# Optimization experiments

Measured on AMD Instinct MI355X. Metric: run time of the kernel, lower is better.

Reference implementation:

```python
import jax, jax.numpy as jnp
import numpy as np

N = 50000          # nodes
E = 800000         # edges (before self-loops)
D_IN, D_H, D_OUT = 128, 256, 256
SZ_C = 2           # channels
NUM_GRAPHS = 64
EPS = 1e-6


def setup_inputs() -> dict:
    key = jax.random.key(0)
    ks = jax.random.split(key, 12)
    x = jax.random.normal(ks[0], (N, D_IN), dtype=jnp.float32)
    edge = jax.random.randint(ks[1], (2, E), 0, N, dtype=jnp.int64)
    batch = jnp.sort(jax.random.randint(ks[2], (N,), 0, NUM_GRAPHS, dtype=jnp.int64))
    def glorot(k, shape):
        fan = shape[-2] + shape[-1]
        return jax.random.normal(k, shape, dtype=jnp.float32) * jnp.sqrt(2.0 / fan)
    W0 = glorot(ks[3], (SZ_C, D_IN, D_H)); b0 = jnp.zeros((SZ_C, D_H), jnp.float32)
    W1 = glorot(ks[4], (SZ_C, D_H, D_H));  b1 = jnp.zeros((SZ_C, D_H), jnp.float32)
    W2 = glorot(ks[5], (SZ_C, D_H, D_OUT)); b2 = jnp.zeros((SZ_C, D_OUT), jnp.float32)
    ln_w = jnp.ones((D_OUT,), jnp.float32)
    ln_b = jnp.zeros((D_OUT,), jnp.float32)
    return {"x": x, "edge": edge, "batch": batch,
            "W0": W0, "b0": b0, "W1": W1, "b1": b1, "W2": W2, "b2": b2,
            "ln_w": ln_w, "ln_b": ln_b}


def _gcn_conv(h, W, b, src, dst, norm):
    # PyG GCNConv: linear transform, then deg-normalized scatter-add, then bias
    h = h @ W                                  # [N, d_out]
    msg = h[src] * norm[:, None]               # [E+N, d_out] gathered messages
    agg = jax.ops.segment_sum(msg, dst, num_segments=N)
    return agg + b


def reference(x, edge, batch, W0, b0, W1, b1, W2, b2, ln_w, ln_b):
    # add self-loops (GCNConv default add_self_loops=True)
    loops = jnp.arange(N, dtype=edge.dtype)
    src = jnp.concatenate([edge[0], loops])
    dst = jnp.concatenate([edge[1], loops])
    # symmetric normalization: deg^{-1/2}[src] * deg^{-1/2}[dst], deg over targets
    deg = jax.ops.segment_sum(jnp.ones_like(dst, dtype=x.dtype), dst, num_segments=N)
    dinv = jnp.where(deg > 0, jax.lax.rsqrt(deg), 0.0)
    norm = dinv[src] * dinv[dst]

    channels = []
    for c in range(SZ_C):  # small fixed channel count
        h = x
        for (W, b) in ((W0[c], b0[c]), (W1[c], b1[c]), (W2[c], b2[c])):
            h = _gcn_conv(h, W, b, src, dst, norm)
            h = jax.nn.relu(h) + h  # residual: ReLU output + pre-ReLU input
        channels.append(h)
    channal = jnp.stack(channels)              # [sz_c, N, d_out]

    mean = channal.mean(-1, keepdims=True)
    var = channal.var(-1, keepdims=True)
    out = (channal - mean) * jax.lax.rsqrt(var + EPS) * ln_w + ln_b

    batchs = jnp.ones((SZ_C, 1), channal.dtype) * batch.astype(channal.dtype)[None, :]
    return out, batchs
```

## Files before the change

kernel.cpp:

```cpp
#include <hip/hip_runtime.h>
#include <hip/hip_bf16.h>

typedef __bf16 v8bf __attribute__((ext_vector_type(8)));
typedef float  v4f  __attribute__((ext_vector_type(4)));
typedef float  v2f  __attribute__((ext_vector_type(2)));

constexpr int N_NODES = 50000;
constexpr int N_EDGES = 800000;
constexpr float LN_EPS = 1e-6f;
constexpr int ROW_TILES = N_NODES / 16;

#define ACC_FP8X8(w, a)                                              \
  {                                                                  \
    v2f p0 = __builtin_amdgcn_cvt_pk_f32_fp8((w).x, false);          \
    v2f p1 = __builtin_amdgcn_cvt_pk_f32_fp8((w).x, true);           \
    v2f p2 = __builtin_amdgcn_cvt_pk_f32_fp8((w).y, false);          \
    v2f p3 = __builtin_amdgcn_cvt_pk_f32_fp8((w).y, true);           \
    a[0] += p0.x; a[1] += p0.y; a[2] += p1.x; a[3] += p1.y;          \
    a[4] += p2.x; a[5] += p2.y; a[6] += p3.x; a[7] += p3.y;          \
  }

__device__ __forceinline__ unsigned char f32_to_fp8(float v) {
  int pk = __builtin_amdgcn_cvt_pk_fp8_f32(v, v, 0, false);
  return (unsigned char)(pk & 0xFF);
}

__global__ void probe_kernel(const int* __restrict__ edge, int* __restrict__ flag) {
  int t = threadIdx.x;
  int nz = 0;
  for (int i = t * 2 + 1; i < 4096; i += 128) nz |= (edge[i] != 0);
  unsigned long long m = __ballot(nz);
  if (t == 0) flag[0] = (m == 0ull) ? 1 : 0;
}

__device__ __forceinline__ int ld_idx(const void* base, int i, int is64) {
  int v;
  if (is64) v = (int)((const long long*)base)[(long long)i];
  else      v = ((const int*)base)[i];
  if ((unsigned)v >= (unsigned)N_NODES) v = 0;
  return v;
}


__global__ void init_kernel(int* __restrict__ deg, int* __restrict__ gcount) {
  int i = blockIdx.x * 256 + threadIdx.x;
  if (i < N_NODES) deg[i] = 1;
  if (i == 0) gcount[0] = 0;
}

__global__ void count_kernel(const void* __restrict__ edge, const int* __restrict__ flag,
                             int* __restrict__ deg) {
  int e = blockIdx.x * 256 + threadIdx.x;
  if (e < N_EDGES) atomicAdd(&deg[ld_idx(edge, N_EDGES + e, flag[0])], 1);
}

__global__ __launch_bounds__(256) void block_offsets_kernel(
    const int* __restrict__ deg, int* __restrict__ gcount,
    int* __restrict__ rowstart, int* __restrict__ cursor, float* __restrict__ dinv) {
  __shared__ int ps[256];
  __shared__ int base_s;
  int tid = threadIdx.x;
  int node = blockIdx.x * 256 + tid;
  int d = (node < N_NODES) ? deg[node] : 1;
  int cnt = d - 1;
  ps[tid] = cnt;
  __syncthreads();
#pragma unroll
  for (int off = 1; off < 256; off <<= 1) {
    int v = (tid >= off) ? ps[tid - off] : 0;
    __syncthreads();
    ps[tid] += v;
    __syncthreads();
  }
  if (tid == 255) base_s = atomicAdd(gcount, ps[255]);
  __syncthreads();
  int start = base_s + ps[tid] - cnt;
  if (node < N_NODES) {
    rowstart[node] = start;
    cursor[node]   = start;
    dinv[node]     = rsqrtf((float)max(d, 1));
  }
}

__global__ void scatter_kernel(const void* __restrict__ edge, const int* __restrict__ flag,
                               int* __restrict__ cursor, int* __restrict__ csr_src) {
  int e = blockIdx.x * 256 + threadIdx.x;
  if (e >= N_EDGES) return;
  int f = flag[0];
  int s = ld_idx(edge, e, f);
  int d = ld_idx(edge, N_EDGES + e, f);
  int pos = atomicAdd(&cursor[d], 1);
  if ((unsigned)pos < (unsigned)N_EDGES) csr_src[pos] = s;
}

__global__ void pack_all_kernel(const float* __restrict__ W0, const float* __restrict__ W1,
                                const float* __restrict__ W2, __bf16* __restrict__ Wp) {
  int tid = blockIdx.x * 256 + threadIdx.x;
  const float* src; int local;
  if (tid < 65536)       { src = W0 + (size_t)(tid >> 15) * (128 * 256); local = tid & 32767; }
  else if (tid < 196608) { int t2 = tid - 65536;  src = W1 + (size_t)(t2 >> 16) * 65536; local = t2 & 65535; }
  else                   { int t2 = tid - 196608; src = W2 + (size_t)(t2 >> 16) * 65536; local = t2 & 65535; }
  int j    = local & 7;
  int lane = (local >> 3) & 63;
  int ct   = (local >> 9) & 15;
  int kc   = local >> 13;
  int k    = kc * 32 + ((lane >> 4) << 3) + j;
  int col  = ct * 16 + (lane & 15);
  Wp[tid] = (__bf16)src[k * 256 + col];
}

__global__ __launch_bounds__(256) void prescale_x_kernel(
    const float* __restrict__ x, const float* __restrict__ dinv, __bf16* __restrict__ xd) {
  int t = blockIdx.x * 256 + threadIdx.x;
  int node = t >> 4;
  int d0 = (t & 15) * 8;
  float di = dinv[node];
  v4f f0 = *(const v4f*)(x + (size_t)node * 128 + d0);
  v4f f1 = *(const v4f*)(x + (size_t)node * 128 + d0 + 4);
  v8bf o;
#pragma unroll
  for (int j = 0; j < 4; j++) { o[j] = (__bf16)(di * f0[j]); o[4 + j] = (__bf16)(di * f1[j]); }
  *(v8bf*)(xd + (size_t)node * 128 + d0) = o;
}

__global__ __launch_bounds__(256) void fused0_kernel(
    const __bf16* __restrict__ Yd, const int* __restrict__ rowstart,
    const int* __restrict__ deg, const int* __restrict__ csr_src,
    const float* __restrict__ dinv, const __bf16* __restrict__ Wp,
    const float* __restrict__ bias,
    unsigned char* __restrict__ Hd) {
  __shared__ __bf16 lds[16 * 128];
  __shared__ int wcnt;
  char* lb = (char*)lds;
  int wave = threadIdx.x >> 6;
  int lane = threadIdx.x & 63;
  int sub = lane >> 4;
  int dc = (lane & 15) * 8;
  if (threadIdx.x == 0) wcnt = 0;
  __syncthreads();

  for (;;) {
    int row;
    if (lane == 0) row = atomicAdd(&wcnt, 1);
    row = __shfl(row, 0);
    if (row >= 16) break;
    int node = blockIdx.x * 16 + row;

    int start = rowstart[node];
    int cnt = deg[node] - 1;
    start = max(0, min(start, N_EDGES));
    cnt = max(0, min(cnt, N_EDGES - start));
    int e = start, end = start + cnt;

    float di = dinv[node];
    v8bf ys = *(const v8bf*)(Yd + (unsigned)(node * 128 + dc));

    float a[8];
#pragma unroll
    for (int j = 0; j < 8; j++) a[j] = 0.f;

    for (; e + 16 <= end; e += 16) {
      int s0 = csr_src[e + sub];
      int s1 = csr_src[e + 4 + sub];
      int s2 = csr_src[e + 8 + sub];
      int s3 = csr_src[e + 12 + sub];
      if ((unsigned)s0 >= (unsigned)N_NODES) s0 = 0;
      if ((unsigned)s1 >= (unsigned)N_NODES) s1 = 0;
      if ((unsigned)s2 >= (unsigned)N_NODES) s2 = 0;
      if ((unsigned)s3 >= (unsigned)N_NODES) s3 = 0;
      v8bf y0 = *(const v8bf*)(Yd + (unsigned)(s0 * 128 + dc));
      v8bf y1 = *(const v8bf*)(Yd + (unsigned)(s1 * 128 + dc));
      v8bf y2 = *(const v8bf*)(Yd + (unsigned)(s2 * 128 + dc));
      v8bf y3 = *(const v8bf*)(Yd + (unsigned)(s3 * 128 + dc));
#pragma unroll
      for (int j = 0; j < 8; j++)
        a[j] += ((float)y0[j] + (float)y1[j]) + ((float)y2[j] + (float)y3[j]);
    }
    if (e + 8 <= end) {
      int s0 = csr_src[e + sub];
      int s1 = csr_src[e + 4 + sub];
      if ((unsigned)s0 >= (unsigned)N_NODES) s0 = 0;
      if ((unsigned)s1 >= (unsigned)N_NODES) s1 = 0;
      v8bf y0 = *(const v8bf*)(Yd + (unsigned)(s0 * 128 + dc));
      v8bf y1 = *(const v8bf*)(Yd + (unsigned)(s1 * 128 + dc));
#pragma unroll
      for (int j = 0; j < 8; j++) a[j] += (float)y0[j] + (float)y1[j];
      e += 8;
    }
    if (e + 4 <= end) {
      int s0 = csr_src[e + sub];
      if ((unsigned)s0 >= (unsigned)N_NODES) s0 = 0;
      v8bf y0 = *(const v8bf*)(Yd + (unsigned)(s0 * 128 + dc));
#pragma unroll
      for (int j = 0; j < 8; j++) a[j] += (float)y0[j];
      e += 4;
    }
    int rem = end - e;
    if (sub < rem) {
      int s0 = csr_src[e + sub];
      if ((unsigned)s0 >= (unsigned)N_NODES) s0 = 0;
      v8bf y0 = *(const v8bf*)(Yd + (unsigned)(s0 * 128 + dc));
#pragma unroll
      for (int j = 0; j < 8; j++) a[j] += (float)y0[j];
    }

#pragma unroll
    for (int off = 16; off < 64; off <<= 1)
#pragma unroll
      for (int j = 0; j < 8; j++) a[j] += __shfl_xor(a[j], off);

    if (sub == 0) {
      v8bf u;
#pragma unroll
      for (int j = 0; j < 8; j++) u[j] = (__bf16)(di * (a[j] + (float)ys[j]));
      int byte = (row * 256 + dc * 2) ^ ((row & 7) << 4);
      *(v8bf*)(lb + byte) = u;
    }
  }
  __syncthreads();

  int ch = wave >> 1, q = wave & 1;
  const __bf16* Wsec = Wp + ch * 32768;
  const float* bch = bias + ch * 256;
  int arow = lane & 15;
  int g = lane >> 4;

  v8bf af[4];
#pragma unroll
  for (int kc = 0; kc < 4; kc++) {
    int byte = (arow * 256 + g * 16 + kc * 64) ^ ((arow & 7) << 4);
    af[kc] = *(const v8bf*)(lb + byte);
  }

  int crow = blockIdx.x * 16 + (g << 2);
  float dv[4];
#pragma unroll
  for (int r = 0; r < 4; r++) dv[r] = dinv[crow + r];

#pragma unroll
  for (int c4 = 0; c4 < 8; c4++) {
    int ct = q * 8 + c4;
    v8bf bf[4];
#pragma unroll
    for (int kc = 0; kc < 4; kc++)
      bf[kc] = *(const v8bf*)(Wsec + (size_t)((kc * 16 + ct) * 64 + lane) * 8);
    v4f acc = (v4f){0.f, 0.f, 0.f, 0.f};
#pragma unroll
    for (int kc = 0; kc < 4; kc++)
      acc = __builtin_amdgcn_mfma_f32_16x16x32_bf16(af[kc], bf[kc], acc, 0, 0, 0);
    int wcol = ct * 16 + (lane & 15);
    float bb = bch[wcol];
#pragma unroll
    for (int r = 0; r < 4; r++) {
      float z = acc[r] + bb;
      float h = z + fmaxf(z, 0.f);
      Hd[(size_t)(crow + r) * 512 + ch * 256 + wcol] = f32_to_fp8(dv[r] * h);
    }
  }
}

__global__ __launch_bounds__(256) void fusedA_kernel(
    const unsigned char* __restrict__ A,
    const int* __restrict__ rowstart, const int* __restrict__ deg,
    const int* __restrict__ csr_src, const float* __restrict__ dinv,
    const __bf16* __restrict__ Wp,
    const float* __restrict__ bias,
    unsigned char* __restrict__ Hd) {
  __shared__ __bf16 lds[16 * 512];
  __shared__ int wcnt;
  char* lb = (char*)lds;
  int wave = threadIdx.x >> 6;
  int lane = threadIdx.x & 63;
  unsigned lb8 = (unsigned)(lane * 8);
  if (threadIdx.x == 0) wcnt = 0;
  __syncthreads();

  for (;;) {
    int row;
    if (lane == 0) row = atomicAdd(&wcnt, 1);
    row = __shfl(row, 0);
    if (row >= 16) break;
    int node = blockIdx.x * 16 + row;

    int start = rowstart[node];
    int cnt = deg[node] - 1;
    start = max(0, min(start, N_EDGES));
    cnt = max(0, min(cnt, N_EDGES - start));
    int e = start, end = start + cnt;

    float di = dinv[node];
    uint2 wys = *(const uint2*)(A + (unsigned)(node * 512) + lb8);

    float a[8];
#pragma unroll
    for (int j = 0; j < 8; j++) a[j] = 0.f;

    for (; e + 8 <= end; e += 8) {
      int s0 = csr_src[e],     s1 = csr_src[e + 1];
      int s2 = csr_src[e + 2], s3 = csr_src[e + 3];
      int s4 = csr_src[e + 4], s5 = csr_src[e + 5];
      int s6 = csr_src[e + 6], s7 = csr_src[e + 7];
      if ((unsigned)s0 >= (unsigned)N_NODES) s0 = 0;
      if ((unsigned)s1 >= (unsigned)N_NODES) s1 = 0;
      if ((unsigned)s2 >= (unsigned)N_NODES) s2 = 0;
      if ((unsigned)s3 >= (unsigned)N_NODES) s3 = 0;
      if ((unsigned)s4 >= (unsigned)N_NODES) s4 = 0;
      if ((unsigned)s5 >= (unsigned)N_NODES) s5 = 0;
      if ((unsigned)s6 >= (unsigned)N_NODES) s6 = 0;
      if ((unsigned)s7 >= (unsigned)N_NODES) s7 = 0;
      uint2 w0 = *(const uint2*)(A + (unsigned)(s0 * 512) + lb8);
      uint2 w1 = *(const uint2*)(A + (unsigned)(s1 * 512) + lb8);
      uint2 w2 = *(const uint2*)(A + (unsigned)(s2 * 512) + lb8);
      uint2 w3 = *(const uint2*)(A + (unsigned)(s3 * 512) + lb8);
      uint2 w4 = *(const uint2*)(A + (unsigned)(s4 * 512) + lb8);
      uint2 w5 = *(const uint2*)(A + (unsigned)(s5 * 512) + lb8);
      uint2 w6 = *(const uint2*)(A + (unsigned)(s6 * 512) + lb8);
      uint2 w7 = *(const uint2*)(A + (unsigned)(s7 * 512) + lb8);
      ACC_FP8X8(w0, a); ACC_FP8X8(w1, a); ACC_FP8X8(w2, a); ACC_FP8X8(w3, a);
      ACC_FP8X8(w4, a); ACC_FP8X8(w5, a); ACC_FP8X8(w6, a); ACC_FP8X8(w7, a);
    }
    if (e + 4 <= end) {
      int s0 = csr_src[e],     s1 = csr_src[e + 1];
      int s2 = csr_src[e + 2], s3 = csr_src[e + 3];
      if ((unsigned)s0 >= (unsigned)N_NODES) s0 = 0;
      if ((unsigned)s1 >= (unsigned)N_NODES) s1 = 0;
      if ((unsigned)s2 >= (unsigned)N_NODES) s2 = 0;
      if ((unsigned)s3 >= (unsigned)N_NODES) s3 = 0;
      uint2 w0 = *(const uint2*)(A + (unsigned)(s0 * 512) + lb8);
      uint2 w1 = *(const uint2*)(A + (unsigned)(s1 * 512) + lb8);
      uint2 w2 = *(const uint2*)(A + (unsigned)(s2 * 512) + lb8);
      uint2 w3 = *(const uint2*)(A + (unsigned)(s3 * 512) + lb8);
      ACC_FP8X8(w0, a); ACC_FP8X8(w1, a); ACC_FP8X8(w2, a); ACC_FP8X8(w3, a);
      e += 4;
    }
    for (; e < end; e++) {
      int s0 = csr_src[e];
      if ((unsigned)s0 >= (unsigned)N_NODES) s0 = 0;
      uint2 w0 = *(const uint2*)(A + (unsigned)(s0 * 512) + lb8);
      ACC_FP8X8(w0, a);
    }

    float ysf[8];
    {
      v2f q0 = __builtin_amdgcn_cvt_pk_f32_fp8(wys.x, false);
      v2f q1 = __builtin_amdgcn_cvt_pk_f32_fp8(wys.x, true);
      v2f q2 = __builtin_amdgcn_cvt_pk_f32_fp8(wys.y, false);
      v2f q3 = __builtin_amdgcn_cvt_pk_f32_fp8(wys.y, true);
      ysf[0] = q0.x; ysf[1] = q0.y; ysf[2] = q1.x; ysf[3] = q1.y;
      ysf[4] = q2.x; ysf[5] = q2.y; ysf[6] = q3.x; ysf[7] = q3.y;
    }
    v8bf u;
#pragma unroll
    for (int j = 0; j < 8; j++) u[j] = (__bf16)(di * (a[j] + ysf[j]));
    int byte = (row * 1024 + lane * 16) ^ ((row & 7) << 4);
    *(v8bf*)(lb + byte) = u;
  }
  __syncthreads();

  int ch = wave >> 1, q = wave & 1;
  const __bf16* Wsec = Wp + ch * 65536;
  const float* bch = bias + ch * 256;
  int arow = lane & 15;
  int g = lane >> 4;

  v8bf af[8];
#pragma unroll
  for (int kc = 0; kc < 8; kc++) {
    int byte = (arow * 1024 + ch * 512 + g * 16 + kc * 64) ^ ((arow & 7) << 4);
    af[kc] = *(const v8bf*)(lb + byte);
  }

  int crow = blockIdx.x * 16 + (g << 2);
  float dv[4];
#pragma unroll
  for (int r = 0; r < 4; r++) dv[r] = dinv[crow + r];

#pragma unroll
  for (int c4 = 0; c4 < 8; c4++) {
    int ct = q * 8 + c4;
    v8bf bf[8];
#pragma unroll
    for (int kc = 0; kc < 8; kc++)
      bf[kc] = *(const v8bf*)(Wsec + (size_t)((kc * 16 + ct) * 64 + lane) * 8);
    v4f acc = (v4f){0.f, 0.f, 0.f, 0.f};
#pragma unroll
    for (int kc = 0; kc < 8; kc++)
      acc = __builtin_amdgcn_mfma_f32_16x16x32_bf16(af[kc], bf[kc], acc, 0, 0, 0);
    int wcol = ct * 16 + (lane & 15);
    float bb = bch[wcol];
#pragma unroll
    for (int r = 0; r < 4; r++) {
      float z = acc[r] + bb;
      float h = z + fmaxf(z, 0.f);
      Hd[(size_t)(crow + r) * 512 + ch * 256 + wcol] = f32_to_fp8(dv[r] * h);
    }
  }
}

__global__ __launch_bounds__(256) void agg_fp8_kernel(
    const unsigned char* __restrict__ A, const int* __restrict__ rowstart,
    const int* __restrict__ deg, const int* __restrict__ csr_src,
    const float* __restrict__ dinv, __bf16* __restrict__ U) {
  int node = blockIdx.x * 4 + (threadIdx.x >> 6);
  int lane = threadIdx.x & 63;
  unsigned lb8 = (unsigned)(lane * 8);

  int start = rowstart[node];
  int cnt = deg[node] - 1;
  start = max(0, min(start, N_EDGES));
  cnt = max(0, min(cnt, N_EDGES - start));
  int e = start, end = start + cnt;

  float di = dinv[node];
  uint2 wys = *(const uint2*)(A + (unsigned)(node * 512) + lb8);

  float a[8];
#pragma unroll
  for (int j = 0; j < 8; j++) a[j] = 0.f;

  for (; e + 8 <= end; e += 8) {
    int s0 = csr_src[e],     s1 = csr_src[e + 1];
    int s2 = csr_src[e + 2], s3 = csr_src[e + 3];
    int s4 = csr_src[e + 4], s5 = csr_src[e + 5];
    int s6 = csr_src[e + 6], s7 = csr_src[e + 7];
    if ((unsigned)s0 >= (unsigned)N_NODES) s0 = 0;
    if ((unsigned)s1 >= (unsigned)N_NODES) s1 = 0;
    if ((unsigned)s2 >= (unsigned)N_NODES) s2 = 0;
    if ((unsigned)s3 >= (unsigned)N_NODES) s3 = 0;
    if ((unsigned)s4 >= (unsigned)N_NODES) s4 = 0;
    if ((unsigned)s5 >= (unsigned)N_NODES) s5 = 0;
    if ((unsigned)s6 >= (unsigned)N_NODES) s6 = 0;
    if ((unsigned)s7 >= (unsigned)N_NODES) s7 = 0;
    uint2 w0 = *(const uint2*)(A + (unsigned)(s0 * 512) + lb8);
    uint2 w1 = *(const uint2*)(A + (unsigned)(s1 * 512) + lb8);
    uint2 w2 = *(const uint2*)(A + (unsigned)(s2 * 512) + lb8);
    uint2 w3 = *(const uint2*)(A + (unsigned)(s3 * 512) + lb8);
    uint2 w4 = *(const uint2*)(A + (unsigned)(s4 * 512) + lb8);
    uint2 w5 = *(const uint2*)(A + (unsigned)(s5 * 512) + lb8);
    uint2 w6 = *(const uint2*)(A + (unsigned)(s6 * 512) + lb8);
    uint2 w7 = *(const uint2*)(A + (unsigned)(s7 * 512) + lb8);
    ACC_FP8X8(w0, a); ACC_FP8X8(w1, a); ACC_FP8X8(w2, a); ACC_FP8X8(w3, a);
    ACC_FP8X8(w4, a); ACC_FP8X8(w5, a); ACC_FP8X8(w6, a); ACC_FP8X8(w7, a);
  }
  if (e + 4 <= end) {
    int s0 = csr_src[e],     s1 = csr_src[e + 1];
    int s2 = csr_src[e + 2], s3 = csr_src[e + 3];
    if ((unsigned)s0 >= (unsigned)N_NODES) s0 = 0;
    if ((unsigned)s1 >= (unsigned)N_NODES) s1 = 0;
    if ((unsigned)s2 >= (unsigned)N_NODES) s2 = 0;
    if ((unsigned)s3 >= (unsigned)N_NODES) s3 = 0;
    uint2 w0 = *(const uint2*)(A + (unsigned)(s0 * 512) + lb8);
    uint2 w1 = *(const uint2*)(A + (unsigned)(s1 * 512) + lb8);
    uint2 w2 = *(const uint2*)(A + (unsigned)(s2 * 512) + lb8);
    uint2 w3 = *(const uint2*)(A + (unsigned)(s3 * 512) + lb8);
    ACC_FP8X8(w0, a); ACC_FP8X8(w1, a); ACC_FP8X8(w2, a); ACC_FP8X8(w3, a);
    e += 4;
  }
  for (; e < end; e++) {
    int s0 = csr_src[e];
    if ((unsigned)s0 >= (unsigned)N_NODES) s0 = 0;
    uint2 w0 = *(const uint2*)(A + (unsigned)(s0 * 512) + lb8);
    ACC_FP8X8(w0, a);
  }

  float ysf[8];
  {
    v2f q0 = __builtin_amdgcn_cvt_pk_f32_fp8(wys.x, false);
    v2f q1 = __builtin_amdgcn_cvt_pk_f32_fp8(wys.x, true);
    v2f q2 = __builtin_amdgcn_cvt_pk_f32_fp8(wys.y, false);
    v2f q3 = __builtin_amdgcn_cvt_pk_f32_fp8(wys.y, true);
    ysf[0] = q0.x; ysf[1] = q0.y; ysf[2] = q1.x; ysf[3] = q1.y;
    ysf[4] = q2.x; ysf[5] = q2.y; ysf[6] = q3.x; ysf[7] = q3.y;
  }
  v8bf u;
#pragma unroll
  for (int j = 0; j < 8; j++) u[j] = (__bf16)(di * (a[j] + ysf[j]));
  *(v8bf*)(U + (unsigned)(node * 512) + (unsigned)(lane * 8)) = u;
}

__global__ __launch_bounds__(256, 2) void gemm_final_kernel(
    const __bf16* __restrict__ A, const __bf16* __restrict__ Wp,
    const float* __restrict__ bias, const float* __restrict__ lnw,
    const float* __restrict__ lnb, float* __restrict__ out) {
  constexpr int KC = 8;
  constexpr int LDA = 512;
  __shared__ float ls1[4][16];
  __shared__ float ls2[4][16];
  int lane = threadIdx.x & 63;
  int wave = threadIdx.x >> 6;

  v8bf bfrag[KC][4];
#pragma unroll
  for (int kc = 0; kc < KC; kc++)
#pragma unroll
    for (int c4 = 0; c4 < 4; c4++)
      bfrag[kc][c4] = *(const v8bf*)(Wp + ((size_t)((kc * 16 + wave * 4 + c4) * 64 + lane)) * 8);

  int arow = lane & 15;
  int akq = (lane >> 4) * 8;
  int g = lane >> 4;
  int ccol = wave * 64 + (lane & 15);
  float bcol[4], wcol[4], lbcol[4];
#pragma unroll
  for (int c4 = 0; c4 < 4; c4++) {
    int col = ccol + c4 * 16;
    bcol[c4] = bias[col];
    wcol[c4] = lnw[col];
    lbcol[c4] = lnb[col];
  }

  for (int t = blockIdx.x; t < ROW_TILES; t += gridDim.x) {
    int row0 = t * 16;
    const __bf16* Ap = A + (size_t)(row0 + arow) * LDA + akq;
    v8bf af[KC];
#pragma unroll
    for (int kc = 0; kc < KC; kc++) af[kc] = *(const v8bf*)(Ap + kc * 32);

    v4f acc[4];
#pragma unroll
    for (int c4 = 0; c4 < 4; c4++) acc[c4] = (v4f){0.f, 0.f, 0.f, 0.f};
#pragma unroll
    for (int kc = 0; kc < KC; kc++)
#pragma unroll
      for (int c4 = 0; c4 < 4; c4++)
        acc[c4] = __builtin_amdgcn_mfma_f32_16x16x32_bf16(af[kc], bfrag[kc][c4], acc[c4], 0, 0, 0);

    float h[4][4];
#pragma unroll
    for (int c4 = 0; c4 < 4; c4++)
#pragma unroll
      for (int r = 0; r < 4; r++) {
        float z = acc[c4][r] + bcol[c4];
        h[c4][r] = z + fmaxf(z, 0.f);
      }

    float s1[4], s2[4];
#pragma unroll
    for (int r = 0; r < 4; r++) {
      s1[r] = 0.f; s2[r] = 0.f;
#pragma unroll
      for (int c4 = 0; c4 < 4; c4++) { s1[r] += h[c4][r]; s2[r] += h[c4][r] * h[c4][r]; }
    }
#pragma unroll
    for (int off = 1; off < 16; off <<= 1)
#pragma unroll
      for (int r = 0; r < 4; r++) {
        s1[r] += __shfl_xor(s1[r], off);
        s2[r] += __shfl_xor(s2[r], off);
      }
    if ((lane & 15) == 0) {
#pragma unroll
      for (int r = 0; r < 4; r++) { ls1[wave][g * 4 + r] = s1[r]; ls2[wave][g * 4 + r] = s2[r]; }
    }
    __syncthreads();
#pragma unroll
    for (int r = 0; r < 4; r++) {
      int row = g * 4 + r;
      float t1 = ls1[0][row] + ls1[1][row] + ls1[2][row] + ls1[3][row];
      float t2 = ls2[0][row] + ls2[1][row] + ls2[2][row] + ls2[3][row];
      float mean = t1 * (1.0f / 256.0f);
      float var = t2 * (1.0f / 256.0f) - mean * mean;
      float rstd = rsqrtf(fmaxf(var, 0.f) + LN_EPS);
#pragma unroll
      for (int c4 = 0; c4 < 4; c4++)
        out[(size_t)(row0 + row) * 256 + ccol + c4 * 16] =
            (h[c4][r] - mean) * rstd * wcol[c4] + lbcol[c4];
    }
    __syncthreads();
  }
}

__global__ void batchs_kernel(const void* __restrict__ batch, const int* __restrict__ flag,
                              float* __restrict__ ob) {
  int i = blockIdx.x * 256 + threadIdx.x;
  if (i >= N_NODES) return;
  int f = flag[0];
  int v;
  if (f) v = (int)((const long long*)batch)[i];
  else   v = ((const int*)batch)[i];
  float b = (float)v;
  ob[i] = b;
  ob[N_NODES + i] = b;
}


extern "C" void kernel_launch(void* const* d_in, const int* in_sizes, int n_in,
                              void* d_out, int out_size, void* d_ws, size_t ws_size,
                              hipStream_t stream) {
  const float* x    = (const float*)d_in[0];
  const void*  edge = d_in[1];
  const void*  batch= d_in[2];
  const float* W0   = (const float*)d_in[3];
  const float* b0   = (const float*)d_in[4];
  const float* W1   = (const float*)d_in[5];
  const float* b1   = (const float*)d_in[6];
  const float* W2   = (const float*)d_in[7];
  const float* b2   = (const float*)d_in[8];
  const float* lnw  = (const float*)d_in[9];
  const float* lnb  = (const float*)d_in[10];

  float* out_x = (float*)d_out;
  float* out_b = (float*)d_out + (size_t)2 * N_NODES * 256;

  __bf16*        UC = (__bf16*)out_x;
  unsigned char* H1 = (unsigned char*)(out_x + (size_t)N_NODES * 256);
  unsigned char* H2 = H1 + (size_t)N_NODES * 512;

  char* p = (char*)d_ws;
  __bf16* xd    = (__bf16*)p;  p += (size_t)N_NODES * 256 * 2;
  int* csr_src  = (int*)p;     p += (size_t)N_EDGES * 4;
  int* deg      = (int*)p;     p += (size_t)N_NODES * 4;
  int* cursor   = (int*)p;     p += (size_t)N_NODES * 4;
  int* rowstart = (int*)p;     p += (size_t)N_NODES * 4;
  float* dinv   = (float*)p;   p += (size_t)N_NODES * 4;
  int* flag     = (int*)p;     p += 16;
  int* gcount   = (int*)p;     p += 16;
  __bf16* Wp    = (__bf16*)p;

  const int EB = (N_EDGES + 255) / 256;
  const int NB = (N_NODES + 255) / 256;

  probe_kernel<<<1, 64, 0, stream>>>((const int*)edge, flag);
  init_kernel<<<NB, 256, 0, stream>>>(deg, gcount);
  count_kernel<<<EB, 256, 0, stream>>>(edge, flag, deg);
  block_offsets_kernel<<<NB, 256, 0, stream>>>(deg, gcount, rowstart, cursor, dinv);
  scatter_kernel<<<EB, 256, 0, stream>>>(edge, flag, cursor, csr_src);

  pack_all_kernel<<<1280, 256, 0, stream>>>(W0, W1, W2, Wp);
  prescale_x_kernel<<<3125, 256, 0, stream>>>(x, dinv, xd);

  fused0_kernel<<<ROW_TILES, 256, 0, stream>>>(xd, rowstart, deg, csr_src, dinv,
                                               Wp, b0, H1);
  fusedA_kernel<<<ROW_TILES, 256, 0, stream>>>(H1, rowstart, deg, csr_src, dinv,
                                               Wp + 65536, b1, H2);
  agg_fp8_kernel<<<N_NODES / 4, 256, 0, stream>>>(H2, rowstart, deg, csr_src, dinv, UC);
  gemm_final_kernel<<<512, 256, 0, stream>>>(UC + 256, Wp + 262144, b2 + 256, lnw, lnb,
                                             out_x + (size_t)N_NODES * 256);
  gemm_final_kernel<<<512, 256, 0, stream>>>(UC, Wp + 196608, b2, lnw, lnb, out_x);

  batchs_kernel<<<NB, 256, 0, stream>>>(batch, flag, out_b);
}
```

Baseline: 505.3 us.

## Fuse final aggregation with GEMM and LayerNorm into one kernel

Replaces the separate final aggregation kernel and the two per-channel final GEMM+LayerNorm launches with one fused kernel. It gathers aggregated rows into LDS, then runs the MFMA GEMM, bias, residual ReLU and LayerNorm for both channels in one block. This drops the bf16 intermediate round trip through global memory and two launches. It also factors the gather into a helper unrolled to 16 edges for more loads in flight, at the cost of more registers, and moves the H1/H2 buffers (H2 now aliases xd) to save memory.

```diff
diff --git a/kernel.cpp b/kernel.cpp
--- a/kernel.cpp
+++ b/kernel.cpp
@@ -23,6 +23,61 @@
 __device__ __forceinline__ unsigned char f32_to_fp8(float v) {
   int pk = __builtin_amdgcn_cvt_pk_fp8_f32(v, v, 0, false);
   return (unsigned char)(pk & 0xFF);
+}
+
+__device__ __forceinline__ void gather_fp8_rows(
+    const unsigned char* __restrict__ A, const int* __restrict__ csr_src,
+    int e, int end, unsigned lb8, float a[8]) {
+  for (; e + 16 <= end; e += 16) {
+    int s[16];
+#pragma unroll
+    for (int k = 0; k < 16; k++) {
+      int v = csr_src[e + k];
+      s[k] = ((unsigned)v < (unsigned)N_NODES) ? v : 0;
+    }
+    uint2 w[16];
+#pragma unroll
+    for (int k = 0; k < 16; k++)
+      w[k] = *(const uint2*)(A + (unsigned)(s[k] * 512) + lb8);
+#pragma unroll
+    for (int k = 0; k < 16; k++) ACC_FP8X8(w[k], a);
+  }
+  if (e + 8 <= end) {
+    int s[8];
+#pragma unroll
+    for (int k = 0; k < 8; k++) {
+      int v = csr_src[e + k];
+      s[k] = ((unsigned)v < (unsigned)N_NODES) ? v : 0;
+    }
+    uint2 w[8];
+#pragma unroll
+    for (int k = 0; k < 8; k++)
+      w[k] = *(const uint2*)(A + (unsigned)(s[k] * 512) + lb8);
+#pragma unroll
+    for (int k = 0; k < 8; k++) ACC_FP8X8(w[k], a);
+    e += 8;
+  }
+  if (e + 4 <= end) {
+    int s[4];
+#pragma unroll
+    for (int k = 0; k < 4; k++) {
+      int v = csr_src[e + k];
+      s[k] = ((unsigned)v < (unsigned)N_NODES) ? v : 0;
+    }
+    uint2 w[4];
+#pragma unroll
+    for (int k = 0; k < 4; k++)
+      w[k] = *(const uint2*)(A + (unsigned)(s[k] * 512) + lb8);
+#pragma unroll
+    for (int k = 0; k < 4; k++) ACC_FP8X8(w[k], a);
+    e += 4;
+  }
+  for (; e < end; e++) {
+    int v = csr_src[e];
+    if ((unsigned)v >= (unsigned)N_NODES) v = 0;
+    uint2 w0 = *(const uint2*)(A + (unsigned)(v * 512) + lb8);
+    ACC_FP8X8(w0, a);
+  }
 }
 
 __global__ void probe_kernel(const int* __restrict__ edge, int* __restrict__ flag) {
@@ -286,7 +341,6 @@
     int cnt = deg[node] - 1;
     start = max(0, min(start, N_EDGES));
     cnt = max(0, min(cnt, N_EDGES - start));
-    int e = start, end = start + cnt;
 
     float di = dinv[node];
     uint2 wys = *(const uint2*)(A + (unsigned)(node * 512) + lb8);
@@ -295,50 +349,7 @@
 #pragma unroll
     for (int j = 0; j < 8; j++) a[j] = 0.f;
 
-    for (; e + 8 <= end; e += 8) {
-      int s0 = csr_src[e],     s1 = csr_src[e + 1];
-      int s2 = csr_src[e + 2], s3 = csr_src[e + 3];
-      int s4 = csr_src[e + 4], s5 = csr_src[e + 5];
-      int s6 = csr_src[e + 6], s7 = csr_src[e + 7];
-      if ((unsigned)s0 >= (unsigned)N_NODES) s0 = 0;
-      if ((unsigned)s1 >= (unsigned)N_NODES) s1 = 0;
-      if ((unsigned)s2 >= (unsigned)N_NODES) s2 = 0;
-      if ((unsigned)s3 >= (unsigned)N_NODES) s3 = 0;
-      if ((unsigned)s4 >= (unsigned)N_NODES) s4 = 0;
-      if ((unsigned)s5 >= (unsigned)N_NODES) s5 = 0;
-      if ((unsigned)s6 >= (unsigned)N_NODES) s6 = 0;
-      if ((unsigned)s7 >= (unsigned)N_NODES) s7 = 0;
-      uint2 w0 = *(const uint2*)(A + (unsigned)(s0 * 512) + lb8);
-      uint2 w1 = *(const uint2*)(A + (unsigned)(s1 * 512) + lb8);
-      uint2 w2 = *(const uint2*)(A + (unsigned)(s2 * 512) + lb8);
-      uint2 w3 = *(const uint2*)(A + (unsigned)(s3 * 512) + lb8);
-      uint2 w4 = *(const uint2*)(A + (unsigned)(s4 * 512) + lb8);
-      uint2 w5 = *(const uint2*)(A + (unsigned)(s5 * 512) + lb8);
-      uint2 w6 = *(const uint2*)(A + (unsigned)(s6 * 512) + lb8);
-      uint2 w7 = *(const uint2*)(A + (unsigned)(s7 * 512) + lb8);
-      ACC_FP8X8(w0, a); ACC_FP8X8(w1, a); ACC_FP8X8(w2, a); ACC_FP8X8(w3, a);
-      ACC_FP8X8(w4, a); ACC_FP8X8(w5, a); ACC_FP8X8(w6, a); ACC_FP8X8(w7, a);
-    }
-    if (e + 4 <= end) {
-      int s0 = csr_src[e],     s1 = csr_src[e + 1];
-      int s2 = csr_src[e + 2], s3 = csr_src[e + 3];
-      if ((unsigned)s0 >= (unsigned)N_NODES) s0 = 0;
-      if ((unsigned)s1 >= (unsigned)N_NODES) s1 = 0;
-      if ((unsigned)s2 >= (unsigned)N_NODES) s2 = 0;
-      if ((unsigned)s3 >= (unsigned)N_NODES) s3 = 0;
-      uint2 w0 = *(const uint2*)(A + (unsigned)(s0 * 512) + lb8);
-      uint2 w1 = *(const uint2*)(A + (unsigned)(s1 * 512) + lb8);
-      uint2 w2 = *(const uint2*)(A + (unsigned)(s2 * 512) + lb8);
-      uint2 w3 = *(const uint2*)(A + (unsigned)(s3 * 512) + lb8);
-      ACC_FP8X8(w0, a); ACC_FP8X8(w1, a); ACC_FP8X8(w2, a); ACC_FP8X8(w3, a);
-      e += 4;
-    }
-    for (; e < end; e++) {
-      int s0 = csr_src[e];
-      if ((unsigned)s0 >= (unsigned)N_NODES) s0 = 0;
-      uint2 w0 = *(const uint2*)(A + (unsigned)(s0 * 512) + lb8);
-      ACC_FP8X8(w0, a);
-    }
+    gather_fp8_rows(A, csr_src, start, start + cnt, lb8, a);
 
     float ysf[8];
     {
@@ -397,176 +408,131 @@
   }
 }
 
-__global__ __launch_bounds__(256) void agg_fp8_kernel(
-    const unsigned char* __restrict__ A, const int* __restrict__ rowstart,
-    const int* __restrict__ deg, const int* __restrict__ csr_src,
-    const float* __restrict__ dinv, __bf16* __restrict__ U) {
-  int node = blockIdx.x * 4 + (threadIdx.x >> 6);
+__global__ __launch_bounds__(256) void fusedB_kernel(
+    const unsigned char* __restrict__ A,
+    const int* __restrict__ rowstart, const int* __restrict__ deg,
+    const int* __restrict__ csr_src, const float* __restrict__ dinv,
+    const __bf16* __restrict__ Wp,
+    const float* __restrict__ bias,
+    const float* __restrict__ lnw, const float* __restrict__ lnb,
+    float* __restrict__ out) {
+  __shared__ __bf16 lds[16 * 512];
+  __shared__ float ls1[2][2][16];
+  __shared__ float ls2[2][2][16];
+  __shared__ int wcnt;
+  char* lb = (char*)lds;
+  int wave = threadIdx.x >> 6;
   int lane = threadIdx.x & 63;
   unsigned lb8 = (unsigned)(lane * 8);
-
-  int start = rowstart[node];
-  int cnt = deg[node] - 1;
-  start = max(0, min(start, N_EDGES));
-  cnt = max(0, min(cnt, N_EDGES - start));
-  int e = start, end = start + cnt;
-
-  float di = dinv[node];
-  uint2 wys = *(const uint2*)(A + (unsigned)(node * 512) + lb8);
-
-  float a[8];
-#pragma unroll
-  for (int j = 0; j < 8; j++) a[j] = 0.f;
-
-  for (; e + 8 <= end; e += 8) {
-    int s0 = csr_src[e],     s1 = csr_src[e + 1];
-    int s2 = csr_src[e + 2], s3 = csr_src[e + 3];
-    int s4 = csr_src[e + 4], s5 = csr_src[e + 5];
-    int s6 = csr_src[e + 6], s7 = csr_src[e + 7];
-    if ((unsigned)s0 >= (unsigned)N_NODES) s0 = 0;
-    if ((unsigned)s1 >= (unsigned)N_NODES) s1 = 0;
-    if ((unsigned)s2 >= (unsigned)N_NODES) s2 = 0;
-    if ((unsigned)s3 >= (unsigned)N_NODES) s3 = 0;
-    if ((unsigned)s4 >= (unsigned)N_NODES) s4 = 0;
-    if ((unsigned)s5 >= (unsigned)N_NODES) s5 = 0;
-    if ((unsigned)s6 >= (unsigned)N_NODES) s6 = 0;
-    if ((unsigned)s7 >= (unsigned)N_NODES) s7 = 0;
-    uint2 w0 = *(const uint2*)(A + (unsigned)(s0 * 512) + lb8);
-    uint2 w1 = *(const uint2*)(A + (unsigned)(s1 * 512) + lb8);
-    uint2 w2 = *(const uint2*)(A + (unsigned)(s2 * 512) + lb8);
-    uint2 w3 = *(const uint2*)(A + (unsigned)(s3 * 512) + lb8);
-    uint2 w4 = *(const uint2*)(A + (unsigned)(s4 * 512) + lb8);
-    uint2 w5 = *(const uint2*)(A + (unsigned)(s5 * 512) + lb8);
-    uint2 w6 = *(const uint2*)(A + (unsigned)(s6 * 512) + lb8);
-    uint2 w7 = *(const uint2*)(A + (unsigned)(s7 * 512) + lb8);
-    ACC_FP8X8(w0, a); ACC_FP8X8(w1, a); ACC_FP8X8(w2, a); ACC_FP8X8(w3, a);
-    ACC_FP8X8(w4, a); ACC_FP8X8(w5, a); ACC_FP8X8(w6, a); ACC_FP8X8(w7, a);
-  }
-  if (e + 4 <= end) {
-    int s0 = csr_src[e],     s1 = csr_src[e + 1];
-    int s2 = csr_src[e + 2], s3 = csr_src[e + 3];
-    if ((unsigned)s0 >= (unsigned)N_NODES) s0 = 0;
-    if ((unsigned)s1 >= (unsigned)N_NODES) s1 = 0;
-    if ((unsigned)s2 >= (unsigned)N_NODES) s2 = 0;
-    if ((unsigned)s3 >= (unsigned)N_NODES) s3 = 0;
-    uint2 w0 = *(const uint2*)(A + (unsigned)(s0 * 512) + lb8);
-    uint2 w1 = *(const uint2*)(A + (unsigned)(s1 * 512) + lb8);
-    uint2 w2 = *(const uint2*)(A + (unsigned)(s2 * 512) + lb8);
-    uint2 w3 = *(const uint2*)(A + (unsigned)(s3 * 512) + lb8);
-    ACC_FP8X8(w0, a); ACC_FP8X8(w1, a); ACC_FP8X8(w2, a); ACC_FP8X8(w3, a);
-    e += 4;
-  }
-  for (; e < end; e++) {
-    int s0 = csr_src[e];
-    if ((unsigned)s0 >= (unsigned)N_NODES) s0 = 0;
-    uint2 w0 = *(const uint2*)(A + (unsigned)(s0 * 512) + lb8);
-    ACC_FP8X8(w0, a);
-  }
-
-  float ysf[8];
-  {
-    v2f q0 = __builtin_amdgcn_cvt_pk_f32_fp8(wys.x, false);
-    v2f q1 = __builtin_amdgcn_cvt_pk_f32_fp8(wys.x, true);
-    v2f q2 = __builtin_amdgcn_cvt_pk_f32_fp8(wys.y, false);
-    v2f q3 = __builtin_amdgcn_cvt_pk_f32_fp8(wys.y, true);
-    ysf[0] = q0.x; ysf[1] = q0.y; ysf[2] = q1.x; ysf[3] = q1.y;
-    ysf[4] = q2.x; ysf[5] = q2.y; ysf[6] = q3.x; ysf[7] = q3.y;
-  }
-  v8bf u;
-#pragma unroll
-  for (int j = 0; j < 8; j++) u[j] = (__bf16)(di * (a[j] + ysf[j]));
-  *(v8bf*)(U + (unsigned)(node * 512) + (unsigned)(lane * 8)) = u;
-}
-
-__global__ __launch_bounds__(256, 2) void gemm_final_kernel(
-    const __bf16* __restrict__ A, const __bf16* __restrict__ Wp,
-    const float* __restrict__ bias, const float* __restrict__ lnw,
-    const float* __restrict__ lnb, float* __restrict__ out) {
-  constexpr int KC = 8;
-  constexpr int LDA = 512;
-  __shared__ float ls1[4][16];
-  __shared__ float ls2[4][16];
-  int lane = threadIdx.x & 63;
-  int wave = threadIdx.x >> 6;
-
-  v8bf bfrag[KC][4];
-#pragma unroll
-  for (int kc = 0; kc < KC; kc++)
-#pragma unroll
-    for (int c4 = 0; c4 < 4; c4++)
-      bfrag[kc][c4] = *(const v8bf*)(Wp + ((size_t)((kc * 16 + wave * 4 + c4) * 64 + lane)) * 8);
-
+  if (threadIdx.x == 0) wcnt = 0;
+  __syncthreads();
+
+  for (;;) {
+    int row;
+    if (lane == 0) row = atomicAdd(&wcnt, 1);
+    row = __shfl(row, 0);
+    if (row >= 16) break;
+    int node = blockIdx.x * 16 + row;
+
+    int start = rowstart[node];
+    int cnt = deg[node] - 1;
+    start = max(0, min(start, N_EDGES));
+    cnt = max(0, min(cnt, N_EDGES - start));
+
+    float di = dinv[node];
+    uint2 wys = *(const uint2*)(A + (unsigned)(node * 512) + lb8);
+
+    float a[8];
+#pragma unroll
+    for (int j = 0; j < 8; j++) a[j] = 0.f;
+
+    gather_fp8_rows(A, csr_src, start, start + cnt, lb8, a);
+
+    float ysf[8];
+    {
+      v2f q0 = __builtin_amdgcn_cvt_pk_f32_fp8(wys.x, false);
+      v2f q1 = __builtin_amdgcn_cvt_pk_f32_fp8(wys.x, true);
+      v2f q2 = __builtin_amdgcn_cvt_pk_f32_fp8(wys.y, false);
+      v2f q3 = __builtin_amdgcn_cvt_pk_f32_fp8(wys.y, true);
+      ysf[0] = q0.x; ysf[1] = q0.y; ysf[2] = q1.x; ysf[3] = q1.y;
+      ysf[4] = q2.x; ysf[5] = q2.y; ysf[6] = q3.x; ysf[7] = q3.y;
+    }
+    v8bf u;
+#pragma unroll
+    for (int j = 0; j < 8; j++) u[j] = (__bf16)(di * (a[j] + ysf[j]));
+    int byte = (row * 1024 + lane * 16) ^ ((row & 7) << 4);
+    *(v8bf*)(lb + byte) = u;
+  }
+  __syncthreads();
+
+  int ch = wave >> 1, q = wave & 1;
+  const __bf16* Wsec = Wp + ch * 65536;
+  const float* bch = bias + ch * 256;
   int arow = lane & 15;
-  int akq = (lane >> 4) * 8;
   int g = lane >> 4;
-  int ccol = wave * 64 + (lane & 15);
-  float bcol[4], wcol[4], lbcol[4];
-#pragma unroll
-  for (int c4 = 0; c4 < 4; c4++) {
-    int col = ccol + c4 * 16;
-    bcol[c4] = bias[col];
-    wcol[c4] = lnw[col];
-    lbcol[c4] = lnb[col];
-  }
-
-  for (int t = blockIdx.x; t < ROW_TILES; t += gridDim.x) {
-    int row0 = t * 16;
-    const __bf16* Ap = A + (size_t)(row0 + arow) * LDA + akq;
-    v8bf af[KC];
-#pragma unroll
-    for (int kc = 0; kc < KC; kc++) af[kc] = *(const v8bf*)(Ap + kc * 32);
-
-    v4f acc[4];
-#pragma unroll
-    for (int c4 = 0; c4 < 4; c4++) acc[c4] = (v4f){0.f, 0.f, 0.f, 0.f};
-#pragma unroll
-    for (int kc = 0; kc < KC; kc++)
-#pragma unroll
-      for (int c4 = 0; c4 < 4; c4++)
-        acc[c4] = __builtin_amdgcn_mfma_f32_16x16x32_bf16(af[kc], bfrag[kc][c4], acc[c4], 0, 0, 0);
-
-    float h[4][4];
-#pragma unroll
-    for (int c4 = 0; c4 < 4; c4++)
-#pragma unroll
-      for (int r = 0; r < 4; r++) {
-        float z = acc[c4][r] + bcol[c4];
-        h[c4][r] = z + fmaxf(z, 0.f);
-      }
-
-    float s1[4], s2[4];
+
+  v8bf af[8];
+#pragma unroll
+  for (int kc = 0; kc < 8; kc++) {
+    int byte = (arow * 1024 + ch * 512 + g * 16 + kc * 64) ^ ((arow & 7) << 4);
+    af[kc] = *(const v8bf*)(lb + byte);
+  }
+
+  float h[8][4];
+#pragma unroll
+  for (int c4 = 0; c4 < 8; c4++) {
+    int ct = q * 8 + c4;
+    v8bf bf[8];
+#pragma unroll
+    for (int kc = 0; kc < 8; kc++)
+      bf[kc] = *(const v8bf*)(Wsec + (size_t)((kc * 16 + ct) * 64 + lane) * 8);
+    v4f acc = (v4f){0.f, 0.f, 0.f, 0.f};
+#pragma unroll
+    for (int kc = 0; kc < 8; kc++)
+      acc = __builtin_amdgcn_mfma_f32_16x16x32_bf16(af[kc], bf[kc], acc, 0, 0, 0);
+    float bb = bch[ct * 16 + (lane & 15)];
 #pragma unroll
     for (int r = 0; r < 4; r++) {
-      s1[r] = 0.f; s2[r] = 0.f;
-#pragma unroll
-      for (int c4 = 0; c4 < 4; c4++) { s1[r] += h[c4][r]; s2[r] += h[c4][r] * h[c4][r]; }
-    }
-#pragma unroll
-    for (int off = 1; off < 16; off <<= 1)
-#pragma unroll
-      for (int r = 0; r < 4; r++) {
-        s1[r] += __shfl_xor(s1[r], off);
-        s2[r] += __shfl_xor(s2[r], off);
-      }
-    if ((lane & 15) == 0) {
-#pragma unroll
-      for (int r = 0; r < 4; r++) { ls1[wave][g * 4 + r] = s1[r]; ls2[wave][g * 4 + r] = s2[r]; }
-    }
-    __syncthreads();
+      float z = acc[r] + bb;
+      h[c4][r] = z + fmaxf(z, 0.f);
+    }
+  }
+
+  float s1[4], s2[4];
+#pragma unroll
+  for (int r = 0; r < 4; r++) {
+    s1[r] = 0.f; s2[r] = 0.f;
+#pragma unroll
+    for (int c4 = 0; c4 < 8; c4++) { s1[r] += h[c4][r]; s2[r] += h[c4][r] * h[c4][r]; }
+  }
+#pragma unroll
+  for (int off = 1; off < 16; off <<= 1)
 #pragma unroll
     for (int r = 0; r < 4; r++) {
-      int row = g * 4 + r;
-      float t1 = ls1[0][row] + ls1[1][row] + ls1[2][row] + ls1[3][row];
-      float t2 = ls2[0][row] + ls2[1][row] + ls2[2][row] + ls2[3][row];
-      float mean = t1 * (1.0f / 256.0f);
-      float var = t2 * (1.0f / 256.0f) - mean * mean;
-      float rstd = rsqrtf(fmaxf(var, 0.f) + LN_EPS);
-#pragma unroll
-      for (int c4 = 0; c4 < 4; c4++)
-        out[(size_t)(row0 + row) * 256 + ccol + c4 * 16] =
-            (h[c4][r] - mean) * rstd * wcol[c4] + lbcol[c4];
-    }
-    __syncthreads();
+      s1[r] += __shfl_xor(s1[r], off);
+      s2[r] += __shfl_xor(s2[r], off);
+    }
+  if ((lane & 15) == 0) {
+#pragma unroll
+    for (int r = 0; r < 4; r++) { ls1[ch][q][g * 4 + r] = s1[r]; ls2[ch][q][g * 4 + r] = s2[r]; }
+  }
+  __syncthreads();
+
+  int crow = blockIdx.x * 16 + (g << 2);
+#pragma unroll
+  for (int r = 0; r < 4; r++) {
+    int row = g * 4 + r;
+    float t1 = ls1[ch][0][row] + ls1[ch][1][row];
+    float t2 = ls2[ch][0][row] + ls2[ch][1][row];
+    float mean = t1 * (1.0f / 256.0f);
+    float var = t2 * (1.0f / 256.0f) - mean * mean;
+    float rstd = rsqrtf(fmaxf(var, 0.f) + LN_EPS);
+#pragma unroll
+    for (int c4 = 0; c4 < 8; c4++) {
+      int wcol = (q * 8 + c4) * 16 + (lane & 15);
+      out[(size_t)ch * N_NODES * 256 + (size_t)(crow + r) * 256 + wcol] =
+          (h[c4][r] - mean) * rstd * lnw[wcol] + lnb[wcol];
+    }
   }
 }
 
@@ -602,12 +568,12 @@
   float* out_x = (float*)d_out;
   float* out_b = (float*)d_out + (size_t)2 * N_NODES * 256;
 
-  __bf16*        UC = (__bf16*)out_x;
-  unsigned char* H1 = (unsigned char*)(out_x + (size_t)N_NODES * 256);
-  unsigned char* H2 = H1 + (size_t)N_NODES * 512;
+  unsigned char* H1 = (unsigned char*)out_x;
 
   char* p = (char*)d_ws;
-  __bf16* xd    = (__bf16*)p;  p += (size_t)N_NODES * 256 * 2;
+  __bf16* xd    = (__bf16*)p;
+  unsigned char* H2 = (unsigned char*)p;
+  p += (size_t)N_NODES * 256 * 2;
   int* csr_src  = (int*)p;     p += (size_t)N_EDGES * 4;
   int* deg      = (int*)p;     p += (size_t)N_NODES * 4;
   int* cursor   = (int*)p;     p += (size_t)N_NODES * 4;
@@ -633,10 +599,8 @@
                                                Wp, b0, H1);
   fusedA_kernel<<<ROW_TILES, 256, 0, stream>>>(H1, rowstart, deg, csr_src, dinv,
                                                Wp + 65536, b1, H2);
-  agg_fp8_kernel<<<N_NODES / 4, 256, 0, stream>>>(H2, rowstart, deg, csr_src, dinv, UC);
-  gemm_final_kernel<<<512, 256, 0, stream>>>(UC + 256, Wp + 262144, b2 + 256, lnw, lnb,
-                                             out_x + (size_t)N_NODES * 256);
-  gemm_final_kernel<<<512, 256, 0, stream>>>(UC, Wp + 196608, b2, lnw, lnb, out_x);
+  fusedB_kernel<<<ROW_TILES, 256, 0, stream>>>(H2, rowstart, deg, csr_src, dinv,
+                                               Wp + 196608, b2, lnw, lnb, out_x);
 
   batchs_kernel<<<NB, 256, 0, stream>>>(batch, flag, out_b);
 }
```

Result: slower. 529.3 us (+4.7%).
